# Kernel optimization log

Hardware: AMD Instinct MI355X
Metric: run time of the kernel (lower is better)

Reference implementation:

```python
import jax, jax.numpy as jnp
import numpy as np

NUM_HEADS = 8
D_MODEL = 512
HEAD_DIM = D_MODEL // NUM_HEADS
LN_EPS = 1e-5


def setup_inputs() -> dict:
    key = jax.random.key(0)
    ks = jax.random.split(key, 12)
    B, S = 8, 1024
    P = 2 * S - 1  # relative position length
    s = 0.02
    return {
        "x": jax.random.normal(ks[0], (B, S, D_MODEL), jnp.float32),
        "pos_emb": jax.random.normal(ks[1], (P, D_MODEL), jnp.float32),
        "ln_w": jnp.ones((D_MODEL,), jnp.float32),
        "ln_b": jnp.zeros((D_MODEL,), jnp.float32),
        "Wq": jax.random.normal(ks[2], (D_MODEL, D_MODEL), jnp.float32) * s,
        "bq": jax.random.normal(ks[3], (D_MODEL,), jnp.float32) * s,
        "Wk": jax.random.normal(ks[4], (D_MODEL, D_MODEL), jnp.float32) * s,
        "bk": jax.random.normal(ks[5], (D_MODEL,), jnp.float32) * s,
        "Wv": jax.random.normal(ks[6], (D_MODEL, D_MODEL), jnp.float32) * s,
        "bv": jax.random.normal(ks[7], (D_MODEL,), jnp.float32) * s,
        "Wo": jax.random.normal(ks[8], (D_MODEL, D_MODEL), jnp.float32) * s,
        "bo": jax.random.normal(ks[9], (D_MODEL,), jnp.float32) * s,
        "Wp": jax.random.normal(ks[10], (D_MODEL, D_MODEL), jnp.float32) * s,
        "pos_bias_u": jax.random.normal(ks[11], (D_MODEL,), jnp.float32) * s,
        "pos_bias_v": jax.random.normal(jax.random.fold_in(key, 99), (D_MODEL,), jnp.float32) * s,
    }


def _rel_shift(x):
    # x: [B, H, S, P] -> Transformer-XL relative shift, return [B, H, S, S]
    b, h, s, p = x.shape
    x = jnp.pad(x, ((0, 0), (0, 0), (0, 0), (1, 0)))  # pad one zero column on left
    x = x.reshape(b, h, p + 1, s)[:, :, 1:, :]
    x = x.reshape(b, h, s, p)
    return x[:, :, :, :s]


def reference(x, pos_emb, ln_w, ln_b, Wq, bq, Wk, bk, Wv, bv, Wo, bo, Wp,
              pos_bias_u, pos_bias_v):
    B, S, D = x.shape
    H, hd = NUM_HEADS, HEAD_DIM
    # LayerNorm
    mu = jnp.mean(x, axis=-1, keepdims=True)
    var = jnp.mean(jnp.square(x - mu), axis=-1, keepdims=True)
    h_ = (x - mu) * jax.lax.rsqrt(var + LN_EPS) * ln_w + ln_b
    # Projections (torch Linear: y = x @ W.T + b)
    q = (h_ @ Wq.T + bq).reshape(B, S, H, hd).transpose(0, 2, 1, 3)  # [B,H,S,hd]
    k = (h_ @ Wk.T + bk).reshape(B, S, H, hd).transpose(0, 2, 1, 3)
    v = (h_ @ Wv.T + bv).reshape(B, S, H, hd).transpose(0, 2, 1, 3)
    bias_u = pos_bias_u.reshape(1, H, 1, hd)
    bias_v = pos_bias_v.reshape(1, H, 1, hd)
    content = jnp.einsum('bhqd,bhkd->bhqk', q + bias_u, k)
    # Positional projection: [P, D] -> [H, P, hd]
    p = (pos_emb @ Wp.T).reshape(-1, H, hd).transpose(1, 0, 2)
    pos_score = jnp.einsum('bhqd,hpd->bhqp', q + bias_v, p)
    pos_score = _rel_shift(pos_score)
    scale = 1.0 / np.sqrt(hd).astype(np.float32)
    attn = jax.nn.softmax((content + pos_score) * scale, axis=-1)
    out = jnp.einsum('bhqk,bhkd->bhqd', attn, v)
    out = out.transpose(0, 2, 1, 3).reshape(B, S, D)
    out = out @ Wo.T + bo
    return x + out
```

## Files before the change

### kernel.cpp

```cpp
#include <hip/hip_runtime.h>
#include <hip/hip_bf16.h>


typedef __attribute__((ext_vector_type(8))) short  s16x8;
typedef __attribute__((ext_vector_type(8))) __bf16 bfv8;
typedef __attribute__((ext_vector_type(4))) float  f32x4;
typedef __attribute__((ext_vector_type(4))) unsigned u32x4;

__device__ __forceinline__ float b2f(short s){
  unsigned u = ((unsigned)(unsigned short)s) << 16;
  float f; __builtin_memcpy(&f, &u, 4); return f;
}
__device__ __forceinline__ short f2b(float f){
  unsigned u; __builtin_memcpy(&u, &f, 4);
  u = (u + 0x7fffu + ((u >> 16) & 1u)) >> 16;
  return (short)u;
}
__device__ __forceinline__ unsigned pk2(float lo, float hi){
  __hip_bfloat162 t = __float22bfloat162_rn(make_float2(lo, hi));
  unsigned u; __builtin_memcpy(&u, &t, 4); return u;
}
__device__ __forceinline__ f32x4 MFMA(s16x8 a, s16x8 b, f32x4 c){
  return __builtin_amdgcn_mfma_f32_16x16x32_bf16(
      __builtin_bit_cast(bfv8, a), __builtin_bit_cast(bfv8, b), c, 0, 0, 0);
}
__device__ __forceinline__ void gload_lds16(const void* g, void* l){
  __builtin_amdgcn_global_load_lds(
      (const __attribute__((address_space(1))) void*)g,
      (__attribute__((address_space(3))) void*)l, 16, 0, 0);
}
__device__ __forceinline__ void cvt8(const float* in, short* out, size_t i8){
  f32x4 a = *(const f32x4*)(in + i8*8);
  f32x4 b = *(const f32x4*)(in + i8*8 + 4);
  u32x4 o;
  o[0] = pk2(a[0],a[1]); o[1] = pk2(a[2],a[3]);
  o[2] = pk2(b[0],b[1]); o[3] = pk2(b[2],b[3]);
  *(u32x4*)(out + i8*8) = o;
}

__global__ __launch_bounds__(256) void prep_kernel(
    const float* __restrict__ Wq, const float* __restrict__ Wk,
    const float* __restrict__ Wv, const float* __restrict__ Wo,
    const float* __restrict__ Wp, const float* __restrict__ pos,
    const float* __restrict__ x, const float* __restrict__ lnw, const float* __restrict__ lnb,
    short* __restrict__ wqkv, short* __restrict__ wo, short* __restrict__ wp,
    short* __restrict__ posbf, short* __restrict__ h_bf)
{
  int bid = blockIdx.x, tid = threadIdx.x;
  if(bid < 640){
    int w = bid >> 7;
    size_t i = (size_t)(bid & 127)*256 + tid;
    const float* src; short* dst;
    if(w == 0){ src = Wq; dst = wqkv; }
    else if(w == 1){ src = Wk; dst = wqkv + 262144; }
    else if(w == 2){ src = Wv; dst = wqkv + 524288; }
    else if(w == 3){ src = Wo; dst = wo; }
    else { src = Wp; dst = wp; }
    cvt8(src, dst, i);
  } else if(bid < 1152){
    size_t i = (size_t)(bid - 640)*256 + tid;
    if(i < 131008) cvt8(pos, posbf, i);
  } else {
    int row = (bid - 1152)*4 + (tid >> 6);
    int lane = tid & 63;
    const float* xr = x + (size_t)row*512;
    f32x4 v0 = *(const f32x4*)(xr + lane*8);
    f32x4 v1 = *(const f32x4*)(xr + lane*8 + 4);
    float s  = v0[0]+v0[1]+v0[2]+v0[3]+v1[0]+v1[1]+v1[2]+v1[3];
    float s2 = v0[0]*v0[0]+v0[1]*v0[1]+v0[2]*v0[2]+v0[3]*v0[3]
             + v1[0]*v1[0]+v1[1]*v1[1]+v1[2]*v1[2]+v1[3]*v1[3];
    #pragma unroll
    for(int m=1;m<64;m<<=1){ s += __shfl_xor(s,m); s2 += __shfl_xor(s2,m); }
    float mu = s * (1.0f/512.0f);
    float rs = rsqrtf(s2*(1.0f/512.0f) - mu*mu + 1e-5f);
    float y[8];
    #pragma unroll
    for(int e=0;e<8;e++){
      float xv = (e<4)? v0[e] : v1[e-4];
      int d = lane*8 + e;
      y[e] = (xv - mu)*rs*lnw[d] + lnb[d];
    }
    u32x4 o;
    o[0]=pk2(y[0],y[1]); o[1]=pk2(y[2],y[3]); o[2]=pk2(y[4],y[5]); o[3]=pk2(y[6],y[7]);
    *(u32x4*)(h_bf + (size_t)row*512 + lane*8) = o;
  }
}

__global__ __launch_bounds__(256) void gemm_fused(
    const short* __restrict__ h_bf, const short* __restrict__ wqkv,
    const float* __restrict__ bq, const float* __restrict__ bk, const float* __restrict__ bv,
    const short* __restrict__ posbf, const short* __restrict__ wp,
    short* __restrict__ q_sw, short* __restrict__ k_sw, short* __restrict__ v_sw,
    short* __restrict__ p_sw)
{
  __shared__ __align__(16) short smem[9216];
  short* At = smem;
  short* Bt = smem + 4096;
  int bid = blockIdx.x, tid = threadIdx.x;
  int wave = tid >> 6, lane = tid & 63;
  int quad = lane >> 4, l16 = lane & 15;
  int srow = lane >> 2, scol = (lane & 3)*8;
  if(bid < 768){
    int bx = bid % 12, by = bid / 12;
    int m0 = by*128, n0 = bx*128;
    int wm = wave >> 1, wn = wave & 1;
    f32x4 acc[4][4] = {};
    for(int k0=0; k0<512; k0+=32){
      #pragma unroll
      for(int c=0;c<2;c++){
        int rb = (wave + 4*c)*16;
        gload_lds16(h_bf + (size_t)(m0 + rb + srow)*512 + k0 + scol, At + rb*32);
        gload_lds16(wqkv + (size_t)(n0 + rb + srow)*512 + k0 + scol, Bt + rb*32);
      }
      __syncthreads();
      s16x8 af[4], bfr[4];
      #pragma unroll
      for(int i=0;i<4;i++) af[i]  = *(const s16x8*)(At + (wm*64 + i*16 + l16)*32 + quad*8);
      #pragma unroll
      for(int j=0;j<4;j++) bfr[j] = *(const s16x8*)(Bt + (wn*64 + j*16 + l16)*32 + quad*8);
      #pragma unroll
      for(int i=0;i<4;i++)
        #pragma unroll
        for(int j=0;j<4;j++)
          acc[i][j] = MFMA(af[i], bfr[j], acc[i][j]);
      __syncthreads();
    }
    int seg = bx >> 2;
    int nseg = (bx & 3)*128;
    int bb = by >> 3;
    const float* bsrc = (seg==0)? bq : (seg==1)? bk : bv;
    float bias_j[4];
    #pragma unroll
    for(int j=0;j<4;j++) bias_j[j] = bsrc[nseg + wn*64 + j*16 + l16];
    if(seg < 2){
      short* dst = seg ? k_sw : q_sw;
      #pragma unroll
      for(int h2=0; h2<2; h2++){
        if(wm == h2){
          #pragma unroll
          for(int i=0;i<4;i++){
            int lr = i*16 + quad*4;
            #pragma unroll
            for(int j=0;j<4;j++){
              int cl = wn*64 + j*16 + l16;
              unsigned p01 = pk2(acc[i][j][0]+bias_j[j], acc[i][j][1]+bias_j[j]);
              unsigned p23 = pk2(acc[i][j][2]+bias_j[j], acc[i][j][3]+bias_j[j]);
              smem[(lr+0)*136 + cl] = (short)p01;
              smem[(lr+1)*136 + cl] = (short)(p01>>16);
              smem[(lr+2)*136 + cl] = (short)p23;
              smem[(lr+3)*136 + cl] = (short)(p23>>16);
            }
          }
        }
        __syncthreads();
        #pragma unroll
        for(int it=0; it<4; it++){
          int ci = it*4 + wave;
          int hs = ci >> 2, tb = ci & 3;
          s16x8 vv = *(const s16x8*)(smem + (tb*16 + l16)*136 + hs*32 + quad*8);
          int hh = (nseg>>6) + (hs>>1);
          int tg = ((m0 + h2*64)>>4) + tb;
          size_t chunk = ((size_t)((bb*8 + hh)*64 + tg))*2 + (hs&1);
          *(s16x8*)(dst + chunk*512 + (size_t)lane*8) = vv;
        }
        __syncthreads();
      }
    } else {
      #pragma unroll
      for(int h2=0; h2<2; h2++){
        int jt = by*2 + h2;
        if(wm == h2){
          #pragma unroll
          for(int i=0;i<4;i++){
            int tl = i*16 + quad*4;
            #pragma unroll
            for(int j=0;j<4;j++){
              int dl = wn*64 + j*16 + l16;
              unsigned p01 = pk2(acc[i][j][0]+bias_j[j], acc[i][j][1]+bias_j[j]);
              unsigned p23 = pk2(acc[i][j][2]+bias_j[j], acc[i][j][3]+bias_j[j]);
              unsigned* w2 = (unsigned*)(smem + dl*72 + tl);
              w2[0] = p01; w2[1] = p23;
            }
          }
        }
        __syncthreads();
        #pragma unroll
        for(int it=0; it<4; it++){
          int ci = it*4 + wave;
          int hl = ci>>3, ds = (ci>>1)&3, jk = ci&1;
          s16x8 vv = *(const s16x8*)(smem + (hl*64 + ds*16 + l16)*72 + jk*32 + quad*8);
          int hh = (nseg>>6) + hl;
          size_t chunk = (((size_t)((bb*8 + hh)*16 + jt))*4 + ds)*2 + jk;
          *(s16x8*)(v_sw + chunk*512 + (size_t)lane*8) = vv;
        }
        __syncthreads();
      }
    }
  } else {
    int pid = bid - 768;
    int bx = pid % 8, by = pid / 8;
    int m0 = by*64, n0 = bx*64;
    int wm = wave >> 1, wn = wave & 1;
    f32x4 acc[2][2] = {};
    for(int k0=0; k0<512; k0+=32){
      int rb = wave*16;
      int ra = m0 + rb + srow; if(ra > 2046) ra = 2046;
      gload_lds16(posbf + (size_t)ra*512 + k0 + scol, At + rb*32);
      gload_lds16(wp + (size_t)(n0 + rb + srow)*512 + k0 + scol, Bt + rb*32);
      __syncthreads();
      s16x8 af[2], bfr[2];
      #pragma unroll
      for(int i=0;i<2;i++) af[i]  = *(const s16x8*)(At + (wm*32 + i*16 + l16)*32 + quad*8);
      #pragma unroll
      for(int j=0;j<2;j++) bfr[j] = *(const s16x8*)(Bt + (wn*32 + j*16 + l16)*32 + quad*8);
      #pragma unroll
      for(int i=0;i<2;i++)
        #pragma unroll
        for(int j=0;j<2;j++)
          acc[i][j] = MFMA(af[i], bfr[j], acc[i][j]);
      __syncthreads();
    }
    #pragma unroll
    for(int i=0;i<2;i++){
      int rowb = m0 + wm*32 + i*16 + quad*4;
      #pragma unroll
      for(int j=0;j<2;j++){
        int col = n0 + wn*32 + j*16 + l16;
        int hh = col>>6, ks = (col>>5)&1, qd = (col>>3)&3, e = col&7;
        int rblk = rowb>>4;
        size_t base = ((size_t)(((hh*128+rblk)*2+ks)*64) + qd*16)*8 + e;
        #pragma unroll
        for(int r=0;r<4;r++)
          p_sw[base + (size_t)(quad*4+r)*8] = f2b(acc[i][j][r]);
      }
    }
  }
}

__global__ __launch_bounds__(256, 3) void attn_kernel(
    const short* __restrict__ q_sw, const short* __restrict__ k_sw,
    const short* __restrict__ v_sw, const short* __restrict__ p_sw,
    const float* __restrict__ bu, const float* __restrict__ bvv,
    short* __restrict__ out)
{
  __shared__ __align__(16) float combf[8320];
  int tid = threadIdx.x;
  int wave = tid >> 6, lane = tid & 63, quad = lane >> 4, l16 = lane & 15;
  int h = blockIdx.y, b = blockIdx.z, bh = b*8 + h;
  int qblk = blockIdx.x;
  int iw = qblk*32;
  short* pw = (short*)combf + wave*2304;

  const short* qb = q_sw + (size_t)bh*65536;
  const short* kb = k_sw + (size_t)bh*65536;
  const short* vb = v_sw + (size_t)bh*65536;
  const short* pb = p_sw + (size_t)h*131072;

  s16x8 qu[2][2], qv[2][2];
  #pragma unroll
  for(int s=0;s<2;s++){
    #pragma unroll
    for(int ks=0;ks<2;ks++){
      s16x8 qr = *(const s16x8*)(qb + ((size_t)((qblk*2+s)*2+ks)*64 + lane)*8);
      short tu[8], tv[8];
      #pragma unroll
      for(int e=0;e<8;e++){
        int d = h*64 + ks*32 + quad*8 + e;
        float f = b2f(qr[e]);
        tu[e] = f2b((f + bu[d]) * 0.125f);
        tv[e] = f2b((f + bvv[d]) * 0.125f);
      }
      qu[s][ks] = *(s16x8*)tu; qv[s][ks] = *(s16x8*)tv;
    }
  }

  s16x8 ones;
  #pragma unroll
  for(int e=0;e<8;e++) ones[e] = (short)0x3F80;

  int srcl[4]; bool lo[4];
  #pragma unroll
  for(int r=0;r<4;r++){
    int il = quad*4 + r;
    srcl[r] = quad*16 + ((l16 + 15 - il) & 15);
    lo[r]   = (l16 <= il);
  }

  f32x4 oacc[2][4] = {};
  f32x4 lacc[2] = {};

  #pragma unroll
  for(int t=0; t<4; t++){
    int jt = wave*4 + t;
    int rb0 = (jt*64 - iw + 1008) >> 4;
    f32x4 ps0[5], ps1[5];
    __builtin_amdgcn_s_setprio(1);
    #pragma unroll
    for(int nt=0;nt<6;nt++){
      int rbp = rb0 - 1 + nt;
      s16x8 pf0 = *(const s16x8*)(pb + ((size_t)(rbp*2+0)*64 + lane)*8);
      s16x8 pf1 = *(const s16x8*)(pb + ((size_t)(rbp*2+1)*64 + lane)*8);
      if(nt >= 1){
        f32x4 a = {};
        a = MFMA(qv[0][0], pf0, a);
        a = MFMA(qv[0][1], pf1, a);
        ps0[nt-1] = a;
      }
      if(nt <= 4){
        f32x4 a = {};
        a = MFMA(qv[1][0], pf0, a);
        a = MFMA(qv[1][1], pf1, a);
        ps1[nt] = a;
      }
    }
    __builtin_amdgcn_s_setprio(0);
    float rot0[4][5], rot1[4][5];
    #pragma unroll
    for(int r=0;r<4;r++){
      #pragma unroll
      for(int nt=0;nt<5;nt++){
        rot0[r][nt] = __shfl(ps0[nt][r], srcl[r]);
        rot1[r][nt] = __shfl(ps1[nt][r], srcl[r]);
      }
    }
    #pragma unroll
    for(int js=0;js<4;js++){
      s16x8 kf0 = *(const s16x8*)(kb + ((size_t)((jt*4+js)*2+0)*64 + lane)*8);
      s16x8 kf1 = *(const s16x8*)(kb + ((size_t)((jt*4+js)*2+1)*64 + lane)*8);
      int col = js*16 + l16;
      {
        f32x4 c0;
        #pragma unroll
        for(int r=0;r<4;r++) c0[r] = lo[r] ? rot0[r][js] : rot0[r][js+1];
        f32x4 a = MFMA(qu[0][0], kf0, c0);
        a = MFMA(qu[0][1], kf1, a);
        unsigned p01 = pk2(__expf(a[0]), __expf(a[1]));
        unsigned p23 = pk2(__expf(a[2]), __expf(a[3]));
        pw[(quad*4+0)*72 + col] = (short)p01;
        pw[(quad*4+1)*72 + col] = (short)(p01>>16);
        pw[(quad*4+2)*72 + col] = (short)p23;
        pw[(quad*4+3)*72 + col] = (short)(p23>>16);
      }
      {
        f32x4 c0;
        #pragma unroll
        for(int r=0;r<4;r++) c0[r] = lo[r] ? rot1[r][js] : rot1[r][js+1];
        f32x4 a = MFMA(qu[1][0], kf0, c0);
        a = MFMA(qu[1][1], kf1, a);
        unsigned p01 = pk2(__expf(a[0]), __expf(a[1]));
        unsigned p23 = pk2(__expf(a[2]), __expf(a[3]));
        pw[1152 + (quad*4+0)*72 + col] = (short)p01;
        pw[1152 + (quad*4+1)*72 + col] = (short)(p01>>16);
        pw[1152 + (quad*4+2)*72 + col] = (short)p23;
        pw[1152 + (quad*4+3)*72 + col] = (short)(p23>>16);
      }
    }
    __builtin_amdgcn_s_setprio(1);
    #pragma unroll
    for(int jk=0;jk<2;jk++){
      s16x8 pa0 = *(const s16x8*)(pw + l16*72 + jk*32 + quad*8);
      s16x8 pa1 = *(const s16x8*)(pw + 1152 + l16*72 + jk*32 + quad*8);
      lacc[0] = MFMA(pa0, ones, lacc[0]);
      lacc[1] = MFMA(pa1, ones, lacc[1]);
      #pragma unroll
      for(int ds=0;ds<4;ds++){
        s16x8 vf = *(const s16x8*)(vb + ((size_t)((jt*4+ds)*2+jk)*64 + lane)*8);
        oacc[0][ds] = MFMA(pa0, vf, oacc[0][ds]);
        oacc[1][ds] = MFMA(pa1, vf, oacc[1][ds]);
      }
    }
    __builtin_amdgcn_s_setprio(0);
  }
  __syncthreads();
  float* comb  = combf;
  float* lcomb = combf + 8192;
  #pragma unroll
  for(int s=0;s<2;s++){
    #pragma unroll
    for(int e=0;e<16;e++) comb[wave*2048 + s*1024 + e*64 + lane] = oacc[s][e>>2][e&3];
    if(l16 == 0){
      #pragma unroll
      for(int r=0;r<4;r++) lcomb[wave*32 + s*16 + quad*4 + r] = lacc[s][r];
    }
  }
  __syncthreads();
  #pragma unroll
  for(int i=0;i<8;i++){
    int v = i*256 + tid;
    int lsrc = v & 63;
    int e = (v >> 6) & 15;
    int s = v >> 10;
    int ds = e >> 2, rr = e & 3;
    int il = (lsrc >> 4)*4 + rr;
    int dim = ds*16 + (lsrc & 15);
    float o = comb[v] + comb[2048+v] + comb[4096+v] + comb[6144+v];
    float l = lcomb[s*16+il] + lcomb[32+s*16+il] + lcomb[64+s*16+il] + lcomb[96+s*16+il];
    float rl = __builtin_amdgcn_rcpf(l);
    out[((size_t)(b*1024 + iw + s*16 + il)*512) + h*64 + dim] = f2b(o * rl);
  }
}

__global__ __launch_bounds__(256) void gemm_out(
    const short* __restrict__ A, const short* __restrict__ B,
    const float* __restrict__ bias, const float* __restrict__ resid,
    float* __restrict__ Cout)
{
  __shared__ __align__(16) short At[64*32];
  __shared__ __align__(16) short Bt[64*32];
  int tid = threadIdx.x;
  int wave = tid >> 6, lane = tid & 63;
  int quad = lane >> 4, l16 = lane & 15;
  int wm = wave >> 1, wn = wave & 1;
  int m0 = blockIdx.y*64, n0 = blockIdx.x*64;
  int srow = lane >> 2, scol = (lane & 3)*8;
  f32x4 acc[2][2] = {};
  for(int k0=0; k0<512; k0+=32){
    int rb = wave*16;
    gload_lds16(A + (size_t)(m0 + rb + srow)*512 + k0 + scol, At + rb*32);
    gload_lds16(B + (size_t)(n0 + rb + srow)*512 + k0 + scol, Bt + rb*32);
    __syncthreads();
    s16x8 af[2], bfr[2];
    #pragma unroll
    for(int i=0;i<2;i++) af[i]  = *(const s16x8*)(At + (wm*32 + i*16 + l16)*32 + quad*8);
    #pragma unroll
    for(int j=0;j<2;j++) bfr[j] = *(const s16x8*)(Bt + (wn*32 + j*16 + l16)*32 + quad*8);
    #pragma unroll
    for(int i=0;i<2;i++)
      #pragma unroll
      for(int j=0;j<2;j++)
        acc[i][j] = MFMA(af[i], bfr[j], acc[i][j]);
    __syncthreads();
  }
  #pragma unroll
  for(int i=0;i<2;i++){
    int rowb = m0 + wm*32 + i*16 + quad*4;
    #pragma unroll
    for(int j=0;j<2;j++){
      int col = n0 + wn*32 + j*16 + l16;
      float bv = bias[col];
      #pragma unroll
      for(int r=0;r<4;r++){
        size_t idx = (size_t)(rowb + r)*512 + col;
        Cout[idx] = acc[i][j][r] + bv + resid[idx];
      }
    }
  }
}

extern "C" void kernel_launch(void* const* d_in, const int* in_sizes, int n_in,
                              void* d_out, int out_size, void* d_ws, size_t ws_size,
                              hipStream_t stream)
{
  const float* x    = (const float*)d_in[0];
  const float* pos  = (const float*)d_in[1];
  const float* lnw  = (const float*)d_in[2];
  const float* lnb  = (const float*)d_in[3];
  const float* Wq   = (const float*)d_in[4];
  const float* bq   = (const float*)d_in[5];
  const float* Wk   = (const float*)d_in[6];
  const float* bk   = (const float*)d_in[7];
  const float* Wv   = (const float*)d_in[8];
  const float* bv   = (const float*)d_in[9];
  const float* Wo   = (const float*)d_in[10];
  const float* bo   = (const float*)d_in[11];
  const float* Wp   = (const float*)d_in[12];
  const float* pbu  = (const float*)d_in[13];
  const float* pbv  = (const float*)d_in[14];
  float* out = (float*)d_out;

  char* ws = (char*)d_ws;
  short* h_bf    = (short*)(ws);
  short* q_sw    = (short*)(ws + ( 8u<<20));
  short* k_sw    = (short*)(ws + (16u<<20));
  short* v_sw    = (short*)(ws + (24u<<20));
  short* a_bf    = (short*)(ws + (32u<<20));
  short* p_sw    = (short*)(ws + (40u<<20));
  short* pos_bf  = (short*)(ws + (42u<<20));
  short* wqkv_bf = (short*)(ws + (44u<<20));
  short* wo_bf   = (short*)(ws + (47u<<20));
  short* wp_bf   = (short*)(ws + (47u<<20) + (512u<<10));

  prep_kernel<<<dim3(3200), 256, 0, stream>>>(Wq, Wk, Wv, Wo, Wp, pos,
                                              x, lnw, lnb,
                                              wqkv_bf, wo_bf, wp_bf, pos_bf, h_bf);
  gemm_fused<<<dim3(1024), 256, 0, stream>>>(h_bf, wqkv_bf, bq, bk, bv,
                                             pos_bf, wp_bf,
                                             q_sw, k_sw, v_sw, p_sw);
  attn_kernel<<<dim3(32,8,8), 256, 0, stream>>>(q_sw, k_sw, v_sw, p_sw, pbu, pbv, a_bf);
  gemm_out<<<dim3(8,128), 256, 0, stream>>>(a_bf, wo_bf, bo, x, out);
  (void)in_sizes; (void)n_in; (void)out_size; (void)ws_size;
}
```

Before: 202.2 us.

## Share K/V tiles across waves via double-buffered LDS and drop cross-wave reduction

The attention kernel changes its split. Before, each block's four waves divided the key range for one 32-row query block and then reduced partial outputs through shared memory. Now each wave owns its own 32-row query block and walks all keys. K/V tiles are staged into double-buffered LDS with async global-to-LDS loads that all four waves share, and positional fragments are prefetched into registers one tile ahead. This removes the final cross-wave combine and the redundant per-wave global K/V reads. In exchange it uses more registers and LDS (occupancy hint lowered from 3 to 2), launches four times fewer blocks, and adds barriers every tile.

```diff
diff --git a/kernel.cpp b/kernel.cpp
--- a/kernel.cpp
+++ b/kernel.cpp
@@ -237,19 +237,21 @@
   }
 }
 
-__global__ __launch_bounds__(256, 3) void attn_kernel(
+__global__ __launch_bounds__(256, 2) void attn_kernel(
     const short* __restrict__ q_sw, const short* __restrict__ k_sw,
     const short* __restrict__ v_sw, const short* __restrict__ p_sw,
     const float* __restrict__ bu, const float* __restrict__ bvv,
     short* __restrict__ out)
 {
-  __shared__ __align__(16) float combf[8320];
+  __shared__ __align__(16) short kv[2][8192];
+  __shared__ __align__(16) short pwall[9216];
   int tid = threadIdx.x;
   int wave = tid >> 6, lane = tid & 63, quad = lane >> 4, l16 = lane & 15;
   int h = blockIdx.y, b = blockIdx.z, bh = b*8 + h;
-  int qblk = blockIdx.x;
-  int iw = qblk*32;
-  short* pw = (short*)combf + wave*2304;
+  int qt = blockIdx.x;
+  int iblk32 = qt*4 + wave;
+  int iw = iblk32*32;
+  short* pw = pwall + wave*2304;
 
   const short* qb = q_sw + (size_t)bh*65536;
   const short* kb = k_sw + (size_t)bh*65536;
@@ -261,7 +263,7 @@
   for(int s=0;s<2;s++){
     #pragma unroll
     for(int ks=0;ks<2;ks++){
-      s16x8 qr = *(const s16x8*)(qb + ((size_t)((qblk*2+s)*2+ks)*64 + lane)*8);
+      s16x8 qr = *(const s16x8*)(qb + ((size_t)((iblk32*2+s)*2+ks)*64 + lane)*8);
       short tu[8], tv[8];
       #pragma unroll
       for(int e=0;e<8;e++){
@@ -288,18 +290,31 @@
 
   f32x4 oacc[2][4] = {};
   f32x4 lacc[2] = {};
-
-  #pragma unroll
-  for(int t=0; t<4; t++){
-    int jt = wave*4 + t;
+  s16x8 Pa[6][2];
+
+  auto STAGE = [&](int jt, int bufi){
+    const short* base = (wave < 2) ? kb : vb;
+    #pragma unroll
+    for(int r=0;r<4;r++){
+      int unit = wave*4 + r;
+      gload_lds16(base + (size_t)jt*4096 + (unit&7)*512 + lane*8,
+                  &kv[bufi][unit*512]);
+    }
+  };
+  auto LOADPOS = [&](int jt){
     int rb0 = (jt*64 - iw + 1008) >> 4;
+    #pragma unroll
+    for(int nt=0;nt<6;nt++)
+      #pragma unroll
+      for(int ks=0;ks<2;ks++)
+        Pa[nt][ks] = *(const s16x8*)(pb + (size_t)((rb0-1+nt)*2+ks)*512 + lane*8);
+  };
+  auto COMPUTE = [&](const short* Kt, const short* Vt, int next_jt){
     f32x4 ps0[5], ps1[5];
     __builtin_amdgcn_s_setprio(1);
     #pragma unroll
     for(int nt=0;nt<6;nt++){
-      int rbp = rb0 - 1 + nt;
-      s16x8 pf0 = *(const s16x8*)(pb + ((size_t)(rbp*2+0)*64 + lane)*8);
-      s16x8 pf1 = *(const s16x8*)(pb + ((size_t)(rbp*2+1)*64 + lane)*8);
+      s16x8 pf0 = Pa[nt][0], pf1 = Pa[nt][1];
       if(nt >= 1){
         f32x4 a = {};
         a = MFMA(qv[0][0], pf0, a);
@@ -314,6 +329,7 @@
       }
     }
     __builtin_amdgcn_s_setprio(0);
+    if(next_jt < 16) LOADPOS(next_jt);
     float rot0[4][5], rot1[4][5];
     #pragma unroll
     for(int r=0;r<4;r++){
@@ -325,8 +341,8 @@
     }
     #pragma unroll
     for(int js=0;js<4;js++){
-      s16x8 kf0 = *(const s16x8*)(kb + ((size_t)((jt*4+js)*2+0)*64 + lane)*8);
-      s16x8 kf1 = *(const s16x8*)(kb + ((size_t)((jt*4+js)*2+1)*64 + lane)*8);
+      s16x8 kf0 = *(const s16x8*)(Kt + (js*2+0)*512 + lane*8);
+      s16x8 kf1 = *(const s16x8*)(Kt + (js*2+1)*512 + lane*8);
       int col = js*16 + l16;
       {
         f32x4 c0;
@@ -364,39 +380,40 @@
       lacc[1] = MFMA(pa1, ones, lacc[1]);
       #pragma unroll
       for(int ds=0;ds<4;ds++){
-        s16x8 vf = *(const s16x8*)(vb + ((size_t)((jt*4+ds)*2+jk)*64 + lane)*8);
+        s16x8 vf = *(const s16x8*)(Vt + (ds*2+jk)*512 + lane*8);
         oacc[0][ds] = MFMA(pa0, vf, oacc[0][ds]);
         oacc[1][ds] = MFMA(pa1, vf, oacc[1][ds]);
       }
     }
     __builtin_amdgcn_s_setprio(0);
-  }
+  };
+
+  STAGE(0, 0);
+  LOADPOS(0);
   __syncthreads();
-  float* comb  = combf;
-  float* lcomb = combf + 8192;
+
+  #pragma unroll 1
+  for(int jt2=0; jt2<8; ++jt2){
+    int jt = jt2*2;
+    STAGE(jt+1, 1);
+    COMPUTE(&kv[0][0], &kv[0][4096], jt+1);
+    __syncthreads();
+    if(jt2 < 7) STAGE(jt+2, 0);
+    COMPUTE(&kv[1][0], &kv[1][4096], jt+2);
+    __syncthreads();
+  }
+
   #pragma unroll
   for(int s=0;s<2;s++){
-    #pragma unroll
-    for(int e=0;e<16;e++) comb[wave*2048 + s*1024 + e*64 + lane] = oacc[s][e>>2][e&3];
-    if(l16 == 0){
-      #pragma unroll
-      for(int r=0;r<4;r++) lcomb[wave*32 + s*16 + quad*4 + r] = lacc[s][r];
-    }
-  }
-  __syncthreads();
-  #pragma unroll
-  for(int i=0;i<8;i++){
-    int v = i*256 + tid;
-    int lsrc = v & 63;
-    int e = (v >> 6) & 15;
-    int s = v >> 10;
-    int ds = e >> 2, rr = e & 3;
-    int il = (lsrc >> 4)*4 + rr;
-    int dim = ds*16 + (lsrc & 15);
-    float o = comb[v] + comb[2048+v] + comb[4096+v] + comb[6144+v];
-    float l = lcomb[s*16+il] + lcomb[32+s*16+il] + lcomb[64+s*16+il] + lcomb[96+s*16+il];
-    float rl = __builtin_amdgcn_rcpf(l);
-    out[((size_t)(b*1024 + iw + s*16 + il)*512) + h*64 + dim] = f2b(o * rl);
+    float rl[4];
+    #pragma unroll
+    for(int r=0;r<4;r++) rl[r] = __builtin_amdgcn_rcpf(lacc[s][r]);
+    #pragma unroll
+    for(int ds=0; ds<4; ds++)
+      #pragma unroll
+      for(int r=0;r<4;r++)
+        out[((size_t)(b*1024 + iw + s*16 + quad*4 + r))*512 + h*64 + ds*16 + l16] =
+            f2b(oacc[s][ds][r] * rl[r]);
   }
 }
 
@@ -486,7 +503,7 @@
   gemm_fused<<<dim3(1024), 256, 0, stream>>>(h_bf, wqkv_bf, bq, bk, bv,
                                              pos_bf, wp_bf,
                                              q_sw, k_sw, v_sw, p_sw);
-  attn_kernel<<<dim3(32,8,8), 256, 0, stream>>>(q_sw, k_sw, v_sw, p_sw, pbu, pbv, a_bf);
+  attn_kernel<<<dim3(8,8,8), 256, 0, stream>>>(q_sw, k_sw, v_sw, p_sw, pbu, pbv, a_bf);
   gemm_out<<<dim3(8,128), 256, 0, stream>>>(a_bf, wo_bf, bo, x, out);
   (void)in_sizes; (void)n_in; (void)out_size; (void)ws_size;
 }
```

Result: faster. 194.0 us (-4.1%).
